# Kernel optimization log

Measured on AMD Instinct MI355X. Metric: run time of the kernel, lower is better.

The kernel has to match this reference:

```python
import jax, jax.numpy as jnp
import numpy as np

B, T, D, N = 32, 512, 1024, 1024


def setup_inputs() -> dict:
    key = jax.random.key(0)
    k1, k2, k3, k4, k5 = jax.random.split(key, 5)
    x = jax.random.normal(k1, (B, T, D), dtype=jnp.float32)
    h0 = jnp.zeros((B, N), dtype=jnp.float32)  # self.h Variable init
    # GRUCell params: gate kernel [D+N, 2N], candidate kernel [D+N, N]
    Wg = jax.random.normal(k2, (D + N, 2 * N), dtype=jnp.float32) * 0.05
    bg = jax.random.normal(k3, (2 * N,), dtype=jnp.float32) * 0.05 + 1.0  # TF gate bias init 1.0
    Wc = jax.random.normal(k4, (D + N, N), dtype=jnp.float32) * 0.05
    bc = jax.random.normal(k5, (N,), dtype=jnp.float32) * 0.05
    return {"x": x, "h0": h0, "Wg": Wg, "bg": bg, "Wc": Wc, "bc": bc}


def reference(x, h0, Wg, bg, Wc, bc):
    # tf.nn.rnn_cell.GRUCell recurrence via dynamic_rnn, single layer
    def step(h, x_t):
        xh = jnp.concatenate([x_t, h], axis=-1)           # [B, D+N]
        gates = jax.nn.sigmoid(xh @ Wg + bg)              # [B, 2N]
        r, u = jnp.split(gates, 2, axis=-1)
        xrh = jnp.concatenate([x_t, r * h], axis=-1)      # [B, D+N]
        c = jnp.tanh(xrh @ Wc + bc)                       # [B, N]
        h_new = u * h + (1.0 - u) * c
        return h_new, h_new

    xs = jnp.swapaxes(x, 0, 1)                            # [T, B, D]
    _, outs = jax.lax.scan(step, h0, xs)                  # outs: [T, B, N]
    outputs = jnp.swapaxes(outs, 0, 1)                    # [B, T, N]
    activations = outputs.reshape(-1, N)                  # [B*T, N]
    return activations
```

## Files before the change

### kernel.cpp

```cpp
#include <hip/hip_runtime.h>
#include <hip/hip_bf16.h>

#define B_ 32
#define T_ 512
#define D_ 1024
#define N_ 1024
#define NWG 192
#define NGATE 128
#define TPB 256
#define SMEM_BYTES (131072 + 16384 + 64)

typedef __attribute__((ext_vector_type(8))) short short8v;
typedef __attribute__((ext_vector_type(4))) float f32x4;

__device__ __forceinline__ float bf2f(unsigned short u) {
  union { float f; unsigned int i; } c; c.i = ((unsigned int)u) << 16; return c.f;
}
__device__ __forceinline__ unsigned short f2bf(float f) {
  union { float f; unsigned int i; } c; c.f = f;
  unsigned int r = c.i + 0x7FFFu + ((c.i >> 16) & 1u);
  return (unsigned short)(r >> 16);
}
__device__ __forceinline__ unsigned cvtpk(float a, float b) {
  unsigned r;
  asm("v_cvt_pk_bf16_f32 %0, %1, %2" : "=v"(r) : "v"(a), "v"(b));
  return r;
}
__device__ __forceinline__ short8v pack_frag(f32x4 lo, f32x4 hi) {
  union { unsigned u[4]; short8v s; } c;
  c.u[0] = cvtpk(lo[0], lo[1]); c.u[1] = cvtpk(lo[2], lo[3]);
  c.u[2] = cvtpk(hi[0], hi[1]); c.u[3] = cvtpk(hi[2], hi[3]);
  return c.s;
}

__device__ __forceinline__ void st_bf16_sc(unsigned short* p, unsigned short v) {
  asm volatile("global_store_short %0, %1, off sc0 sc1"
               :: "v"((unsigned long long)p), "v"((unsigned)v) : "memory");
}
__device__ __forceinline__ void st_f32_sc(float* p, float v) {
  asm volatile("global_store_dword %0, %1, off sc0 sc1"
               :: "v"((unsigned long long)p), "v"(v) : "memory");
}

__device__ __forceinline__ void flag_store(unsigned* line, unsigned v) {
  __hip_atomic_store(line, v, __ATOMIC_RELAXED, __HIP_MEMORY_SCOPE_AGENT);
}
__device__ __forceinline__ void poll2(const unsigned* p0, bool a0,
                                      const unsigned* p1, bool a1, unsigned tgt) {
  int tries = 0;
  for (;;) {
    unsigned v0 = tgt, v1 = tgt;
    if (a0) v0 = __hip_atomic_load(p0, __ATOMIC_RELAXED, __HIP_MEMORY_SCOPE_AGENT);
    if (a1) v1 = __hip_atomic_load(p1, __ATOMIC_RELAXED, __HIP_MEMORY_SCOPE_AGENT);
    if (__all((int)(v0 >= tgt && v1 >= tgt))) break;
    __builtin_amdgcn_s_sleep(1);
    if (++tries > (1 << 20)) break;
  }
}

__device__ __forceinline__ int frag_off(int m, int k) {
  const int mt = m >> 4, ks = k >> 5, kk = k & 31;
  const int l = (m & 15) + (((kk >> 2) & 3) << 4);
  const int j = (kk & 3) + ((kk >> 4) << 2);
  return ((mt * 32 + ks) * 64 + l) * 8 + j;
}

template <int KS>
__device__ __forceinline__ void build_xfrags(const float* __restrict__ x, int t,
                                             int kbase, int lane,
                                             short8v frag[2][KS]) {
#pragma unroll
  for (int mt = 0; mt < 2; ++mt) {
    const int m = mt * 16 + (lane & 15);
    const float* row = x + ((size_t)m * T_ + t) * D_;
#pragma unroll
    for (int ks = 0; ks < KS; ++ks) {
      const int k0 = kbase + ks * 32 + ((lane >> 4) << 2);
      f32x4 lo = *(const f32x4*)(row + k0);
      f32x4 hi = *(const f32x4*)(row + k0 + 16);
      frag[mt][ks] = pack_frag(lo, hi);
    }
  }
}

template <int KS>
__device__ __forceinline__ void mfma_reg(const short8v frag[2][KS],
                                         const unsigned short* __restrict__ ldsW,
                                         int ksg0, f32x4* acc, int lane) {
#pragma unroll
  for (int mt = 0; mt < 2; ++mt)
#pragma unroll
    for (int ks = 0; ks < KS; ++ks) {
      const int ksg = ksg0 + ks;
      short8v bhi = *(const short8v*)(ldsW + ((size_t)(0 * 64 + ksg) * 64 + lane) * 8);
      short8v blo = *(const short8v*)(ldsW + ((size_t)(1 * 64 + ksg) * 64 + lane) * 8);
      acc[mt] = __builtin_amdgcn_mfma_f32_16x16x32_bf16(frag[mt][ks], bhi, acc[mt], 0, 0, 0);
      acc[mt] = __builtin_amdgcn_mfma_f32_16x16x32_bf16(frag[mt][ks], blo, acc[mt], 0, 0, 0);
    }
}

__global__ __launch_bounds__(TPB, 1) void gru_persistent(
    const float* __restrict__ x, const float* __restrict__ h0,
    const float* __restrict__ Wg, const float* __restrict__ bg,
    const float* __restrict__ Wc, const float* __restrict__ bc,
    float* __restrict__ out,
    unsigned* __restrict__ ctrs,
    unsigned short* __restrict__ hq,
    unsigned short* __restrict__ rhq,
    float* __restrict__ u_buf,
    float* __restrict__ h_buf)
{
  const int wg = blockIdx.x;
  const int tid = threadIdx.x;
  const int lane = tid & 63;
  const int wv = tid >> 6;

  extern __shared__ char smem[];
  unsigned short* ldsW = (unsigned short*)smem;
  float* ldsR = (float*)(smem + 131072);
  float* ldsBias = (float*)(smem + 131072 + 16384);

  unsigned* flagH = ctrs;
  unsigned* flagG = ctrs + 256 * 16;

  const bool is_gate = wg < NGATE;
  const int c0 = (is_gate ? wg : (wg - NGATE)) * 16;
  const float* Wsrc = is_gate ? Wg : Wc;
  const int ldw = is_gate ? 2 * N_ : N_;
  const float* bias = is_gate ? bg : bc;

  const int col = tid & 15, row = tid >> 4;
  const int colg = c0 + col;
  const int b0 = row, b1 = 16 + row;

  for (int i = tid; i < 64 * 64; i += TPB) {
    const int ks = i >> 6, l = i & 63;
    const int n = l & 15, kqp = (l >> 4) * 4;
#pragma unroll
    for (int j = 0; j < 8; ++j) {
      const int k = ks * 32 + ((j < 4) ? 0 : 16) + kqp + (j & 3);
      const float w = Wsrc[(size_t)k * ldw + c0 + n];
      const unsigned short hi = f2bf(w);
      const unsigned short lo = f2bf(w - bf2f(hi));
      ldsW[((size_t)(0 * 64 + ks) * 64 + l) * 8 + j] = hi;
      ldsW[((size_t)(1 * 64 + ks) * 64 + l) * 8 + j] = lo;
    }
  }
  if (tid < 16) ldsBias[tid] = bias[c0 + tid];
  __syncthreads();

  if (is_gate) {
    const bool r_wg = (c0 < N_);
    unsigned* wflag = flagG + (size_t)(wg * 4 + wv) * 16;
    const unsigned* pp = flagH + (size_t)((16 * wv + (lane >> 2)) * 4 + (lane & 3)) * 16;
    const unsigned* pe = flagH + (size_t)(wg * 4 + wv) * 16;
    const bool ae = r_wg && (lane == 0);

    f32x4 accA[2] = {{0.f,0.f,0.f,0.f},{0.f,0.f,0.f,0.f}};
    {
      short8v xf[2][8];
      build_xfrags<8>(x, 0, wv * 256, lane, xf);
      mfma_reg<8>(xf, ldsW, wv * 8, accA, lane);
    }
    for (int t = 0; t < T_; ++t) {
      poll2(pp, true, pe, ae, (unsigned)(t + 1));
      const unsigned short* hqr = hq + (((t + 1) & 1) << 15);
      float hv0 = 0.f, hv1 = 0.f;
      if (r_wg)
        asm volatile("global_load_dword %0, %2, off sc0 sc1\n\t"
                     "global_load_dword %1, %3, off sc0 sc1"
                     : "=&v"(hv0), "=&v"(hv1)
                     : "v"((unsigned long long)(h_buf + b0 * N_ + colg)),
                       "v"((unsigned long long)(h_buf + b1 * N_ + colg))
                     : "memory");
      short8v areg[2][8];
#pragma unroll
      for (int mt = 0; mt < 2; ++mt)
#pragma unroll
        for (int ks = 0; ks < 8; ++ks) {
          const unsigned short* p =
              hqr + ((size_t)((mt * 32 + wv * 8 + ks) * 64 + lane)) * 8;
          asm volatile("global_load_dwordx4 %0, %1, off sc0 sc1"
                       : "=v"(areg[mt][ks]) : "v"((unsigned long long)p) : "memory");
        }
      asm volatile("s_waitcnt vmcnt(0)" ::: "memory");
      __builtin_amdgcn_sched_barrier(0);
#pragma unroll
      for (int mt = 0; mt < 2; ++mt)
#pragma unroll
        for (int ks = 0; ks < 8; ++ks) {
          const int ksg = 32 + wv * 8 + ks;
          short8v bhi = *(const short8v*)(ldsW + ((size_t)(0 * 64 + ksg) * 64 + lane) * 8);
          short8v blo = *(const short8v*)(ldsW + ((size_t)(1 * 64 + ksg) * 64 + lane) * 8);
          accA[mt] = __builtin_amdgcn_mfma_f32_16x16x32_bf16(areg[mt][ks], bhi, accA[mt], 0, 0, 0);
          accA[mt] = __builtin_amdgcn_mfma_f32_16x16x32_bf16(areg[mt][ks], blo, accA[mt], 0, 0, 0);
        }
      float* ldsRp = ldsR + (t & 1) * 2048;
#pragma unroll
      for (int mt = 0; mt < 2; ++mt)
#pragma unroll
        for (int r = 0; r < 4; ++r)
          ldsRp[(wv * 2 + mt) * 256 + (4 * (lane >> 4) + r) * 16 + (lane & 15)] = accA[mt][r];
      __syncthreads();
      {
        float s0 = ldsRp[0 * 256 + tid] + ldsRp[2 * 256 + tid]
                 + ldsRp[4 * 256 + tid] + ldsRp[6 * 256 + tid];
        float s1 = ldsRp[1 * 256 + tid] + ldsRp[3 * 256 + tid]
                 + ldsRp[5 * 256 + tid] + ldsRp[7 * 256 + tid];
        float p0 = fminf(fmaxf(s0 + ldsBias[col], -30.f), 30.f);
        float p1 = fminf(fmaxf(s1 + ldsBias[col], -30.f), 30.f);
        const float g0 = 1.f / (1.f + __expf(-p0));
        const float g1 = 1.f / (1.f + __expf(-p1));
        if (r_wg) {
          st_bf16_sc(rhq + frag_off(b0, colg), f2bf(g0 * hv0));
          st_bf16_sc(rhq + frag_off(b1, colg), f2bf(g1 * hv1));
        } else {
          st_f32_sc(u_buf + b0 * N_ + (colg - N_), g0);
          st_f32_sc(u_buf + b1 * N_ + (colg - N_), g1);
        }
      }
      asm volatile("s_waitcnt vmcnt(0)" ::: "memory");
      if (lane == 0) flag_store(wflag, (unsigned)(t + 1));
      if (t + 1 < T_) {
        accA[0] = (f32x4){0.f,0.f,0.f,0.f};
        accA[1] = (f32x4){0.f,0.f,0.f,0.f};
        short8v xf[2][8];
        build_xfrags<8>(x, t + 1, wv * 256, lane, xf);
        mfma_reg<8>(xf, ldsW, wv * 8, accA, lane);
      }
    }
  } else {
    const int cidx = wg - NGATE;
    unsigned* wflag = flagH + (size_t)(cidx * 4 + wv) * 16;
    const unsigned* pp1 = flagG + (size_t)((16 * wv + (lane >> 2)) * 4 + (lane & 3)) * 16;
    const unsigned* pe1 = flagG + (size_t)((64 + cidx) * 4 + (lane & 3)) * 16;
    const bool ae1 = (lane < 4);

    float hreg0 = h0[b0 * N_ + colg];
    float hreg1 = h0[b1 * N_ + colg];
    st_f32_sc(h_buf + b0 * N_ + colg, hreg0);
    st_f32_sc(h_buf + b1 * N_ + colg, hreg1);
    st_bf16_sc(hq + 32768 + frag_off(b0, colg), f2bf(hreg0));
    st_bf16_sc(hq + 32768 + frag_off(b1, colg), f2bf(hreg1));
    asm volatile("s_waitcnt vmcnt(0)" ::: "memory");
    if (lane == 0) flag_store(wflag, 1u);

    f32x4 accA[2] = {{0.f,0.f,0.f,0.f},{0.f,0.f,0.f,0.f}};
    {
      short8v xf[2][8];
      build_xfrags<8>(x, 0, wv * 256, lane, xf);
      mfma_reg<8>(xf, ldsW, wv * 8, accA, lane);
    }
    for (int t = 0; t < T_; ++t) {
      poll2(pp1, true, pe1, ae1, (unsigned)(t + 1));
      float uv0, uv1;
      asm volatile("global_load_dword %0, %2, off sc0 sc1\n\t"
                   "global_load_dword %1, %3, off sc0 sc1"
                   : "=&v"(uv0), "=&v"(uv1)
                   : "v"((unsigned long long)(u_buf + b0 * N_ + colg)),
                     "v"((unsigned long long)(u_buf + b1 * N_ + colg))
                   : "memory");
      short8v areg[2][8];
#pragma unroll
      for (int mt = 0; mt < 2; ++mt)
#pragma unroll
        for (int ks = 0; ks < 8; ++ks) {
          const unsigned short* p =
              rhq + ((size_t)((mt * 32 + wv * 8 + ks) * 64 + lane)) * 8;
          asm volatile("global_load_dwordx4 %0, %1, off sc0 sc1"
                       : "=v"(areg[mt][ks]) : "v"((unsigned long long)p) : "memory");
        }
      asm volatile("s_waitcnt vmcnt(0)" ::: "memory");
      __builtin_amdgcn_sched_barrier(0);
#pragma unroll
      for (int mt = 0; mt < 2; ++mt)
#pragma unroll
        for (int ks = 0; ks < 8; ++ks) {
          const int ksg = 32 + wv * 8 + ks;
          short8v bhi = *(const short8v*)(ldsW + ((size_t)(0 * 64 + ksg) * 64 + lane) * 8);
          short8v blo = *(const short8v*)(ldsW + ((size_t)(1 * 64 + ksg) * 64 + lane) * 8);
          accA[mt] = __builtin_amdgcn_mfma_f32_16x16x32_bf16(areg[mt][ks], bhi, accA[mt], 0, 0, 0);
          accA[mt] = __builtin_amdgcn_mfma_f32_16x16x32_bf16(areg[mt][ks], blo, accA[mt], 0, 0, 0);
        }
      float* ldsRp = ldsR + (t & 1) * 2048;
#pragma unroll
      for (int mt = 0; mt < 2; ++mt)
#pragma unroll
        for (int r = 0; r < 4; ++r)
          ldsRp[(wv * 2 + mt) * 256 + (4 * (lane >> 4) + r) * 16 + (lane & 15)] = accA[mt][r];
      __syncthreads();
      {
        float s0 = ldsRp[0 * 256 + tid] + ldsRp[2 * 256 + tid]
                 + ldsRp[4 * 256 + tid] + ldsRp[6 * 256 + tid];
        float s1 = ldsRp[1 * 256 + tid] + ldsRp[3 * 256 + tid]
                 + ldsRp[5 * 256 + tid] + ldsRp[7 * 256 + tid];
        float p0 = fminf(fmaxf(s0 + ldsBias[col], -20.f), 20.f);
        float p1v = fminf(fmaxf(s1 + ldsBias[col], -20.f), 20.f);
        const float e0 = __expf(2.f * p0), e1 = __expf(2.f * p1v);
        const float c0v = (e0 - 1.f) / (e0 + 1.f);
        const float c1v = (e1 - 1.f) / (e1 + 1.f);
        const float hn0 = uv0 * hreg0 + (1.f - uv0) * c0v;
        const float hn1 = uv1 * hreg1 + (1.f - uv1) * c1v;
        hreg0 = hn0; hreg1 = hn1;
        unsigned short* hqw = hq + ((t & 1) << 15);
        st_bf16_sc(hqw + frag_off(b0, colg), f2bf(hn0));
        st_bf16_sc(hqw + frag_off(b1, colg), f2bf(hn1));
        st_f32_sc(h_buf + b0 * N_ + colg, hn0);
        st_f32_sc(h_buf + b1 * N_ + colg, hn1);
        out[((size_t)b0 * T_ + t) * N_ + colg] = hn0;
        out[((size_t)b1 * T_ + t) * N_ + colg] = hn1;
      }
      asm volatile("s_waitcnt vmcnt(0)" ::: "memory");
      if (lane == 0) flag_store(wflag, (unsigned)(t + 2));
      if (t + 1 < T_) {
        accA[0] = (f32x4){0.f,0.f,0.f,0.f};
        accA[1] = (f32x4){0.f,0.f,0.f,0.f};
        short8v xf[2][8];
        build_xfrags<8>(x, t + 1, wv * 256, lane, xf);
        mfma_reg<8>(xf, ldsW, wv * 8, accA, lane);
      }
    }
  }
}

extern "C" void kernel_launch(void* const* d_in, const int* in_sizes, int n_in,
                              void* d_out, int out_size, void* d_ws, size_t ws_size,
                              hipStream_t stream) {
  const float* x  = (const float*)d_in[0];
  const float* h0 = (const float*)d_in[1];
  const float* Wg = (const float*)d_in[2];
  const float* bg = (const float*)d_in[3];
  const float* Wc = (const float*)d_in[4];
  const float* bc = (const float*)d_in[5];
  float* out = (float*)d_out;

  char* w = (char*)d_ws;
  unsigned* ctrs       = (unsigned*)(w + 0);
  unsigned short* hq   = (unsigned short*)(w + 49152);
  unsigned short* rhq  = (unsigned short*)(w + 180224);
  float* u_buf         = (float*)(w + 245760);
  float* h_buf         = (float*)(w + 376832);

  hipFuncSetAttribute((const void*)gru_persistent,
                      hipFuncAttributeMaxDynamicSharedMemorySize, SMEM_BYTES);
  hipMemsetAsync(w, 0, 49152, stream);
  gru_persistent<<<NWG, TPB, SMEM_BYTES, stream>>>(
      x, h0, Wg, bg, Wc, bc, out, ctrs, hq, rhq, u_buf, h_buf);
}
```

Baseline: 3.198 ms.

## Split work by batch rows per wave to drop LDS cross-wave K reduction

Workgroups shrink from four waves to two. Each wave now owns 16 batch rows and the full K range instead of a quarter of K for all 32 rows. This removes the LDS partial-sum buffer, the per-step __syncthreads and the cross-wave reduction, and each wave finishes its own gate or candidate math and signals its own flag. The cost is twice the serial MFMA chain per wave (32 k-steps), with split accumulators to keep independent chains, higher register pressure from 32 A-fragments, and fewer waves to hide latency.

```diff
diff --git a/kernel.cpp b/kernel.cpp
--- a/kernel.cpp
+++ b/kernel.cpp
@@ -7,8 +7,8 @@
 #define N_ 1024
 #define NWG 192
 #define NGATE 128
-#define TPB 256
-#define SMEM_BYTES (131072 + 16384 + 64)
+#define TPB 128
+#define SMEM_BYTES (131072 + 64)
 
 typedef __attribute__((ext_vector_type(8))) short short8v;
 typedef __attribute__((ext_vector_type(4))) float f32x4;
@@ -65,38 +65,32 @@
   return ((mt * 32 + ks) * 64 + l) * 8 + j;
 }
 
-template <int KS>
-__device__ __forceinline__ void build_xfrags(const float* __restrict__ x, int t,
-                                             int kbase, int lane,
-                                             short8v frag[2][KS]) {
-#pragma unroll
-  for (int mt = 0; mt < 2; ++mt) {
-    const int m = mt * 16 + (lane & 15);
-    const float* row = x + ((size_t)m * T_ + t) * D_;
-#pragma unroll
-    for (int ks = 0; ks < KS; ++ks) {
-      const int k0 = kbase + ks * 32 + ((lane >> 4) << 2);
+__device__ __forceinline__ void shadow_x(const float* __restrict__ x, int t,
+                                         int m16, int lane,
+                                         const unsigned short* __restrict__ ldsW,
+                                         f32x4* acc) {
+  const float* row = x + ((size_t)(m16 + (lane & 15)) * T_ + t) * D_;
+#pragma unroll
+  for (int c = 0; c < 4; ++c) {
+    short8v xf[8];
+#pragma unroll
+    for (int i = 0; i < 8; ++i) {
+      const int ks = c * 8 + i;
+      const int k0 = ks * 32 + ((lane >> 4) << 2);
       f32x4 lo = *(const f32x4*)(row + k0);
       f32x4 hi = *(const f32x4*)(row + k0 + 16);
-      frag[mt][ks] = pack_frag(lo, hi);
-    }
-  }
-}
-
-template <int KS>
-__device__ __forceinline__ void mfma_reg(const short8v frag[2][KS],
-                                         const unsigned short* __restrict__ ldsW,
-                                         int ksg0, f32x4* acc, int lane) {
-#pragma unroll
-  for (int mt = 0; mt < 2; ++mt)
-#pragma unroll
-    for (int ks = 0; ks < KS; ++ks) {
-      const int ksg = ksg0 + ks;
-      short8v bhi = *(const short8v*)(ldsW + ((size_t)(0 * 64 + ksg) * 64 + lane) * 8);
-      short8v blo = *(const short8v*)(ldsW + ((size_t)(1 * 64 + ksg) * 64 + lane) * 8);
-      acc[mt] = __builtin_amdgcn_mfma_f32_16x16x32_bf16(frag[mt][ks], bhi, acc[mt], 0, 0, 0);
-      acc[mt] = __builtin_amdgcn_mfma_f32_16x16x32_bf16(frag[mt][ks], blo, acc[mt], 0, 0, 0);
-    }
+      xf[i] = pack_frag(lo, hi);
+    }
+#pragma unroll
+    for (int i = 0; i < 8; ++i) {
+      const int ks = c * 8 + i;
+      short8v bhi = *(const short8v*)(ldsW + ((size_t)(0 * 64 + ks) * 64 + lane) * 8);
+      short8v blo = *(const short8v*)(ldsW + ((size_t)(1 * 64 + ks) * 64 + lane) * 8);
+      const int a = (ks & 16) ? 2 : 0;
+      acc[a]     = __builtin_amdgcn_mfma_f32_16x16x32_bf16(xf[i], bhi, acc[a], 0, 0, 0);
+      acc[a + 1] = __builtin_amdgcn_mfma_f32_16x16x32_bf16(xf[i], blo, acc[a + 1], 0, 0, 0);
+    }
+  }
 }
 
 __global__ __launch_bounds__(TPB, 1) void gru_persistent(
@@ -117,11 +111,10 @@
 
   extern __shared__ char smem[];
   unsigned short* ldsW = (unsigned short*)smem;
-  float* ldsR = (float*)(smem + 131072);
-  float* ldsBias = (float*)(smem + 131072 + 16384);
+  float* ldsBias = (float*)(smem + 131072);
 
   unsigned* flagH = ctrs;
-  unsigned* flagG = ctrs + 256 * 16;
+  unsigned* flagG = ctrs + 128 * 16;
 
   const bool is_gate = wg < NGATE;
   const int c0 = (is_gate ? wg : (wg - NGATE)) * 16;
@@ -129,9 +122,8 @@
   const int ldw = is_gate ? 2 * N_ : N_;
   const float* bias = is_gate ? bg : bc;
 
-  const int col = tid & 15, row = tid >> 4;
-  const int colg = c0 + col;
-  const int b0 = row, b1 = 16 + row;
+  const int colg = c0 + (lane & 15);
+  const int r0 = wv * 16 + ((lane >> 4) << 2);
 
   for (int i = tid; i < 64 * 64; i += TPB) {
     const int ks = i >> 6, l = i & 63;
@@ -151,173 +143,129 @@
 
   if (is_gate) {
     const bool r_wg = (c0 < N_);
-    unsigned* wflag = flagG + (size_t)(wg * 4 + wv) * 16;
-    const unsigned* pp = flagH + (size_t)((16 * wv + (lane >> 2)) * 4 + (lane & 3)) * 16;
-    const unsigned* pe = flagH + (size_t)(wg * 4 + wv) * 16;
+    unsigned* wflag = flagG + (size_t)(wg * 2 + wv) * 16;
+    const unsigned* pp = flagH + (size_t)(lane * 2 + wv) * 16;
+    const unsigned* pe = flagH + (size_t)(wg * 2 + wv) * 16;
     const bool ae = r_wg && (lane == 0);
 
-    f32x4 accA[2] = {{0.f,0.f,0.f,0.f},{0.f,0.f,0.f,0.f}};
-    {
-      short8v xf[2][8];
-      build_xfrags<8>(x, 0, wv * 256, lane, xf);
-      mfma_reg<8>(xf, ldsW, wv * 8, accA, lane);
-    }
+    f32x4 acc[4] = {{0,0,0,0},{0,0,0,0},{0,0,0,0},{0,0,0,0}};
+    shadow_x(x, 0, wv * 16, lane, ldsW, acc);
+
     for (int t = 0; t < T_; ++t) {
       poll2(pp, true, pe, ae, (unsigned)(t + 1));
       const unsigned short* hqr = hq + (((t + 1) & 1) << 15);
-      float hv0 = 0.f, hv1 = 0.f;
-      if (r_wg)
-        asm volatile("global_load_dword %0, %2, off sc0 sc1\n\t"
-                     "global_load_dword %1, %3, off sc0 sc1"
-                     : "=&v"(hv0), "=&v"(hv1)
-                     : "v"((unsigned long long)(h_buf + b0 * N_ + colg)),
-                       "v"((unsigned long long)(h_buf + b1 * N_ + colg))
-                     : "memory");
-      short8v areg[2][8];
-#pragma unroll
-      for (int mt = 0; mt < 2; ++mt)
-#pragma unroll
-        for (int ks = 0; ks < 8; ++ks) {
-          const unsigned short* p =
-              hqr + ((size_t)((mt * 32 + wv * 8 + ks) * 64 + lane)) * 8;
-          asm volatile("global_load_dwordx4 %0, %1, off sc0 sc1"
-                       : "=v"(areg[mt][ks]) : "v"((unsigned long long)p) : "memory");
-        }
+      float hv[4];
+      if (r_wg) {
+#pragma unroll
+        for (int r = 0; r < 4; ++r)
+          asm volatile("global_load_dword %0, %1, off sc0 sc1"
+                       : "=v"(hv[r])
+                       : "v"((unsigned long long)(h_buf + (size_t)(r0 + r) * N_ + colg))
+                       : "memory");
+      }
+      short8v areg[32];
+#pragma unroll
+      for (int ks = 0; ks < 32; ++ks) {
+        const unsigned short* p = hqr + ((size_t)((wv * 32 + ks) * 64 + lane)) * 8;
+        asm volatile("global_load_dwordx4 %0, %1, off sc0 sc1"
+                     : "=v"(areg[ks]) : "v"((unsigned long long)p) : "memory");
+      }
       asm volatile("s_waitcnt vmcnt(0)" ::: "memory");
       __builtin_amdgcn_sched_barrier(0);
 #pragma unroll
-      for (int mt = 0; mt < 2; ++mt)
-#pragma unroll
-        for (int ks = 0; ks < 8; ++ks) {
-          const int ksg = 32 + wv * 8 + ks;
-          short8v bhi = *(const short8v*)(ldsW + ((size_t)(0 * 64 + ksg) * 64 + lane) * 8);
-          short8v blo = *(const short8v*)(ldsW + ((size_t)(1 * 64 + ksg) * 64 + lane) * 8);
-          accA[mt] = __builtin_amdgcn_mfma_f32_16x16x32_bf16(areg[mt][ks], bhi, accA[mt], 0, 0, 0);
-          accA[mt] = __builtin_amdgcn_mfma_f32_16x16x32_bf16(areg[mt][ks], blo, accA[mt], 0, 0, 0);
-        }
-      float* ldsRp = ldsR + (t & 1) * 2048;
-#pragma unroll
-      for (int mt = 0; mt < 2; ++mt)
-#pragma unroll
-        for (int r = 0; r < 4; ++r)
-          ldsRp[(wv * 2 + mt) * 256 + (4 * (lane >> 4) + r) * 16 + (lane & 15)] = accA[mt][r];
-      __syncthreads();
-      {
-        float s0 = ldsRp[0 * 256 + tid] + ldsRp[2 * 256 + tid]
-                 + ldsRp[4 * 256 + tid] + ldsRp[6 * 256 + tid];
-        float s1 = ldsRp[1 * 256 + tid] + ldsRp[3 * 256 + tid]
-                 + ldsRp[5 * 256 + tid] + ldsRp[7 * 256 + tid];
-        float p0 = fminf(fmaxf(s0 + ldsBias[col], -30.f), 30.f);
-        float p1 = fminf(fmaxf(s1 + ldsBias[col], -30.f), 30.f);
-        const float g0 = 1.f / (1.f + __expf(-p0));
-        const float g1 = 1.f / (1.f + __expf(-p1));
-        if (r_wg) {
-          st_bf16_sc(rhq + frag_off(b0, colg), f2bf(g0 * hv0));
-          st_bf16_sc(rhq + frag_off(b1, colg), f2bf(g1 * hv1));
-        } else {
-          st_f32_sc(u_buf + b0 * N_ + (colg - N_), g0);
-          st_f32_sc(u_buf + b1 * N_ + (colg - N_), g1);
-        }
+      for (int ks = 0; ks < 32; ++ks) {
+        const int ksg = 32 + ks;
+        short8v bhi = *(const short8v*)(ldsW + ((size_t)(0 * 64 + ksg) * 64 + lane) * 8);
+        short8v blo = *(const short8v*)(ldsW + ((size_t)(1 * 64 + ksg) * 64 + lane) * 8);
+        const int a = (ks & 16) ? 2 : 0;
+        acc[a]     = __builtin_amdgcn_mfma_f32_16x16x32_bf16(areg[ks], bhi, acc[a], 0, 0, 0);
+        acc[a + 1] = __builtin_amdgcn_mfma_f32_16x16x32_bf16(areg[ks], blo, acc[a + 1], 0, 0, 0);
+      }
+      f32x4 s4 = (acc[0] + acc[1]) + (acc[2] + acc[3]);
+      const float bcol = ldsBias[lane & 15];
+#pragma unroll
+      for (int r = 0; r < 4; ++r) {
+        float pre = fminf(fmaxf(s4[r] + bcol, -30.f), 30.f);
+        const float g = 1.f / (1.f + __expf(-pre));
+        if (r_wg) st_bf16_sc(rhq + frag_off(r0 + r, colg), f2bf(g * hv[r]));
+        else      st_f32_sc(u_buf + (size_t)(r0 + r) * N_ + (colg - N_), g);
       }
       asm volatile("s_waitcnt vmcnt(0)" ::: "memory");
       if (lane == 0) flag_store(wflag, (unsigned)(t + 1));
       if (t + 1 < T_) {
-        accA[0] = (f32x4){0.f,0.f,0.f,0.f};
-        accA[1] = (f32x4){0.f,0.f,0.f,0.f};
-        short8v xf[2][8];
-        build_xfrags<8>(x, t + 1, wv * 256, lane, xf);
-        mfma_reg<8>(xf, ldsW, wv * 8, accA, lane);
+        acc[0] = (f32x4){0,0,0,0}; acc[1] = (f32x4){0,0,0,0};
+        acc[2] = (f32x4){0,0,0,0}; acc[3] = (f32x4){0,0,0,0};
+        shadow_x(x, t + 1, wv * 16, lane, ldsW, acc);
       }
     }
   } else {
     const int cidx = wg - NGATE;
-    unsigned* wflag = flagH + (size_t)(cidx * 4 + wv) * 16;
-    const unsigned* pp1 = flagG + (size_t)((16 * wv + (lane >> 2)) * 4 + (lane & 3)) * 16;
-    const unsigned* pe1 = flagG + (size_t)((64 + cidx) * 4 + (lane & 3)) * 16;
-    const bool ae1 = (lane < 4);
-
-    float hreg0 = h0[b0 * N_ + colg];
-    float hreg1 = h0[b1 * N_ + colg];
-    st_f32_sc(h_buf + b0 * N_ + colg, hreg0);
-    st_f32_sc(h_buf + b1 * N_ + colg, hreg1);
-    st_bf16_sc(hq + 32768 + frag_off(b0, colg), f2bf(hreg0));
-    st_bf16_sc(hq + 32768 + frag_off(b1, colg), f2bf(hreg1));
+    unsigned* wflag = flagH + (size_t)(cidx * 2 + wv) * 16;
+    const unsigned* pp1 = flagG + (size_t)(lane * 2 + wv) * 16;
+    const unsigned* pe1 = flagG + (size_t)((64 + cidx) * 2 + wv) * 16;
+    const bool ae1 = (lane == 0);
+
+    float hreg[4];
+#pragma unroll
+    for (int r = 0; r < 4; ++r) {
+      hreg[r] = h0[(size_t)(r0 + r) * N_ + colg];
+      st_f32_sc(h_buf + (size_t)(r0 + r) * N_ + colg, hreg[r]);
+      st_bf16_sc(hq + 32768 + frag_off(r0 + r, colg), f2bf(hreg[r]));
+    }
     asm volatile("s_waitcnt vmcnt(0)" ::: "memory");
     if (lane == 0) flag_store(wflag, 1u);
 
-    f32x4 accA[2] = {{0.f,0.f,0.f,0.f},{0.f,0.f,0.f,0.f}};
-    {
-      short8v xf[2][8];
-      build_xfrags<8>(x, 0, wv * 256, lane, xf);
-      mfma_reg<8>(xf, ldsW, wv * 8, accA, lane);
-    }
+    f32x4 acc[4] = {{0,0,0,0},{0,0,0,0},{0,0,0,0},{0,0,0,0}};
+    shadow_x(x, 0, wv * 16, lane, ldsW, acc);
+
     for (int t = 0; t < T_; ++t) {
       poll2(pp1, true, pe1, ae1, (unsigned)(t + 1));
-      float uv0, uv1;
-      asm volatile("global_load_dword %0, %2, off sc0 sc1\n\t"
-                   "global_load_dword %1, %3, off sc0 sc1"
-                   : "=&v"(uv0), "=&v"(uv1)
-                   : "v"((unsigned long long)(u_buf + b0 * N_ + colg)),
-                     "v"((unsigned long long)(u_buf + b1 * N_ + colg))
-                   : "memory");
-      short8v areg[2][8];
-#pragma unroll
-      for (int mt = 0; mt < 2; ++mt)
-#pragma unroll
-        for (int ks = 0; ks < 8; ++ks) {
-          const unsigned short* p =
-              rhq + ((size_t)((mt * 32 + wv * 8 + ks) * 64 + lane)) * 8;
-          asm volatile("global_load_dwordx4 %0, %1, off sc0 sc1"
-                       : "=v"(areg[mt][ks]) : "v"((unsigned long long)p) : "memory");
-        }
+      float uv[4];
+#pragma unroll
+      for (int r = 0; r < 4; ++r)
+        asm volatile("global_load_dword %0, %1, off sc0 sc1"
+                     : "=v"(uv[r])
+                     : "v"((unsigned long long)(u_buf + (size_t)(r0 + r) * N_ + colg))
+                     : "memory");
+      short8v areg[32];
+#pragma unroll
+      for (int ks = 0; ks < 32; ++ks) {
+        const unsigned short* p = rhq + ((size_t)((wv * 32 + ks) * 64 + lane)) * 8;
+        asm volatile("global_load_dwordx4 %0, %1, off sc0 sc1"
+                     : "=v"(areg[ks]) : "v"((unsigned long long)p) : "memory");
+      }
       asm volatile("s_waitcnt vmcnt(0)" ::: "memory");
       __builtin_amdgcn_sched_barrier(0);
 #pragma unroll
-      for (int mt = 0; mt < 2; ++mt)
-#pragma unroll
-        for (int ks = 0; ks < 8; ++ks) {
-          const int ksg = 32 + wv * 8 + ks;
-          short8v bhi = *(const short8v*)(ldsW + ((size_t)(0 * 64 + ksg) * 64 + lane) * 8);
-          short8v blo = *(const short8v*)(ldsW + ((size_t)(1 * 64 + ksg) * 64 + lane) * 8);
-          accA[mt] = __builtin_amdgcn_mfma_f32_16x16x32_bf16(areg[mt][ks], bhi, accA[mt], 0, 0, 0);
-          accA[mt] = __builtin_amdgcn_mfma_f32_16x16x32_bf16(areg[mt][ks], blo, accA[mt], 0, 0, 0);
-        }
-      float* ldsRp = ldsR + (t & 1) * 2048;
-#pragma unroll
-      for (int mt = 0; mt < 2; ++mt)
-#pragma unroll
-        for (int r = 0; r < 4; ++r)
-          ldsRp[(wv * 2 + mt) * 256 + (4 * (lane >> 4) + r) * 16 + (lane & 15)] = accA[mt][r];
-      __syncthreads();
-      {
-        float s0 = ldsRp[0 * 256 + tid] + ldsRp[2 * 256 + tid]
-                 + ldsRp[4 * 256 + tid] + ldsRp[6 * 256 + tid];
-        float s1 = ldsRp[1 * 256 + tid] + ldsRp[3 * 256 + tid]
-                 + ldsRp[5 * 256 + tid] + ldsRp[7 * 256 + tid];
-        float p0 = fminf(fmaxf(s0 + ldsBias[col], -20.f), 20.f);
-        float p1v = fminf(fmaxf(s1 + ldsBias[col], -20.f), 20.f);
-        const float e0 = __expf(2.f * p0), e1 = __expf(2.f * p1v);
-        const float c0v = (e0 - 1.f) / (e0 + 1.f);
-        const float c1v = (e1 - 1.f) / (e1 + 1.f);
-        const float hn0 = uv0 * hreg0 + (1.f - uv0) * c0v;
-        const float hn1 = uv1 * hreg1 + (1.f - uv1) * c1v;
-        hreg0 = hn0; hreg1 = hn1;
-        unsigned short* hqw = hq + ((t & 1) << 15);
-        st_bf16_sc(hqw + frag_off(b0, colg), f2bf(hn0));
-        st_bf16_sc(hqw + frag_off(b1, colg), f2bf(hn1));
-        st_f32_sc(h_buf + b0 * N_ + colg, hn0);
-        st_f32_sc(h_buf + b1 * N_ + colg, hn1);
-        out[((size_t)b0 * T_ + t) * N_ + colg] = hn0;
-        out[((size_t)b1 * T_ + t) * N_ + colg] = hn1;
+      for (int ks = 0; ks < 32; ++ks) {
+        const int ksg = 32 + ks;
+        short8v bhi = *(const short8v*)(ldsW + ((size_t)(0 * 64 + ksg) * 64 + lane) * 8);
+        short8v blo = *(const short8v*)(ldsW + ((size_t)(1 * 64 + ksg) * 64 + lane) * 8);
+        const int a = (ks & 16) ? 2 : 0;
+        acc[a]     = __builtin_amdgcn_mfma_f32_16x16x32_bf16(areg[ks], bhi, acc[a], 0, 0, 0);
+        acc[a + 1] = __builtin_amdgcn_mfma_f32_16x16x32_bf16(areg[ks], blo, acc[a + 1], 0, 0, 0);
+      }
+      f32x4 s4 = (acc[0] + acc[1]) + (acc[2] + acc[3]);
+      const float bcol = ldsBias[lane & 15];
+      unsigned short* hqw = hq + ((t & 1) << 15);
+      float hn[4];
+#pragma unroll
+      for (int r = 0; r < 4; ++r) {
+        float pre = fminf(fmaxf(s4[r] + bcol, -20.f), 20.f);
+        const float e = __expf(2.f * pre);
+        const float cv = (e - 1.f) / (e + 1.f);
+        hn[r] = uv[r] * hreg[r] + (1.f - uv[r]) * cv;
+        hreg[r] = hn[r];
+        st_bf16_sc(hqw + frag_off(r0 + r, colg), f2bf(hn[r]));
+        st_f32_sc(h_buf + (size_t)(r0 + r) * N_ + colg, hn[r]);
+        out[((size_t)(r0 + r) * T_ + t) * N_ + colg] = hn[r];
       }
       asm volatile("s_waitcnt vmcnt(0)" ::: "memory");
       if (lane == 0) flag_store(wflag, (unsigned)(t + 2));
       if (t + 1 < T_) {
-        accA[0] = (f32x4){0.f,0.f,0.f,0.f};
-        accA[1] = (f32x4){0.f,0.f,0.f,0.f};
-        short8v xf[2][8];
-        build_xfrags<8>(x, t + 1, wv * 256, lane, xf);
-        mfma_reg<8>(xf, ldsW, wv * 8, accA, lane);
+        acc[0] = (f32x4){0,0,0,0}; acc[1] = (f32x4){0,0,0,0};
+        acc[2] = (f32x4){0,0,0,0}; acc[3] = (f32x4){0,0,0,0};
+        shadow_x(x, t + 1, wv * 16, lane, ldsW, acc);
       }
     }
   }
@@ -336,14 +284,14 @@
 
   char* w = (char*)d_ws;
   unsigned* ctrs       = (unsigned*)(w + 0);
-  unsigned short* hq   = (unsigned short*)(w + 49152);
-  unsigned short* rhq  = (unsigned short*)(w + 180224);
-  float* u_buf         = (float*)(w + 245760);
-  float* h_buf         = (float*)(w + 376832);
+  unsigned short* hq   = (unsigned short*)(w + 32768);
+  unsigned short* rhq  = (unsigned short*)(w + 163840);
+  float* u_buf         = (float*)(w + 229376);
+  float* h_buf         = (float*)(w + 360448);
 
   hipFuncSetAttribute((const void*)gru_persistent,
                       hipFuncAttributeMaxDynamicSharedMemorySize, SMEM_BYTES);
-  hipMemsetAsync(w, 0, 49152, stream);
+  hipMemsetAsync(w, 0, 32768, stream);
   gru_persistent<<<NWG, TPB, SMEM_BYTES, stream>>>(
       x, h0, Wg, bg, Wc, bc, out, ctrs, hq, rhq, u_buf, h_buf);
 }
```

After: 7.759 ms. 143% more time.
